# Performance work log

Measured on AMD Instinct MI355X. Metric: run time of the kernel, lower is better.

Reference implementation:

```python
import jax, jax.numpy as jnp
import numpy as np

B, P, K, D, T = 512, 64, 8, 512, 50000


def setup_inputs() -> dict:
    key = jax.random.key(0)
    k1, k2, k3, k4, k5, k6 = jax.random.split(key, 6)
    return {
        "inputs": jax.random.normal(k1, (B, P, D), dtype=jnp.float32),
        "title_emb_mat": jax.random.normal(k2, (T, D), dtype=jnp.float32),
        "nbr_batch": jax.random.randint(k3, (B, P, K), 0, B, dtype=jnp.int32),
        "nbr_job": jax.random.randint(k4, (B, P, K), 0, P, dtype=jnp.int32),
        "nbr_title": jax.random.randint(k5, (B, P, K), 0, T, dtype=jnp.int32),
        "nbr_mask": jax.random.randint(k6, (B, P, K), 0, 2, dtype=jnp.int32),
    }


def reference(inputs, title_emb_mat, nbr_batch, nbr_job, nbr_title, nbr_mask):
    # inputs:        [B, P, D]  job embeddings per employee position
    # title_emb_mat: [T, Dt]    title embedding table (Dt == D here)
    # nbr_*:         [B, P, K]  padded metapath neighbor indices + validity mask
    mask = nbr_mask.astype(bool)                              # [B,P,K]
    ref_embs = inputs[nbr_batch, nbr_job]                     # [B,P,K,D] gather of neighbor job embs
    # attention logits: focal emb vs neighbor embs (raw inner product, exp-normalized)
    raw_s = jnp.einsum('bpd,bpkd->bpk', inputs, ref_embs)     # [B,P,K]
    logits = jnp.where(mask, raw_s, jnp.float32(-1e9))
    sim = jax.nn.softmax(logits, axis=-1) * mask              # exact zeros on padded slots;
    # an all-masked (i,pos) -> uniform softmax * 0 mask == 0 row (matches torch 'continue' -> zeros)
    ref_t_embs = title_emb_mat[nbr_title]                     # [B,P,K,Dt] gather of target-title embs
    graph_concat = jnp.einsum('bpk,bpkt->bpt', sim, ref_t_embs)  # [B,P,Dt]
    out = jnp.concatenate([inputs, graph_concat], axis=-1)    # [B,P,D+Dt]
    return out.reshape(B * P, D + title_emb_mat.shape[1])     # torch.cat over batch, axis=0
```

## Files before the change

### kernel.cpp

```cpp
#include <hip/hip_runtime.h>

#define BB 512
#define PP 64
#define KK 8
#define DD 512

typedef float v4f __attribute__((ext_vector_type(4)));

__global__ __launch_bounds__(256) void han_meta_kernel(
    const float* __restrict__ inputs,
    const float* __restrict__ title,
    const int*   __restrict__ nbr_batch,
    const int*   __restrict__ nbr_job,
    const int*   __restrict__ nbr_title,
    const int*   __restrict__ nbr_mask,
    float*       __restrict__ out)
{
    const int lane = threadIdx.x & 63;
    const int wave = threadIdx.x >> 6;
    const int row  = blockIdx.x * 4 + wave;

    const float4* inp4 = (const float4*)(inputs + (size_t)row * DD);
    const float4 fa = inp4[lane];
    const float4 fb = inp4[lane + 64];

    const int4* nb4 = (const int4*)(nbr_batch + row * KK);
    const int4* nj4 = (const int4*)(nbr_job   + row * KK);
    const int4* nt4 = (const int4*)(nbr_title + row * KK);
    const int4* nm4 = (const int4*)(nbr_mask  + row * KK);
    int nbk[KK], njk[KK], ntk[KK], nmk[KK];
    *(int4*)&nbk[0] = nb4[0]; *(int4*)&nbk[4] = nb4[1];
    *(int4*)&njk[0] = nj4[0]; *(int4*)&njk[4] = nj4[1];
    *(int4*)&ntk[0] = nt4[0]; *(int4*)&ntk[4] = nt4[1];
    *(int4*)&nmk[0] = nm4[0]; *(int4*)&nmk[4] = nm4[1];

    float logit[KK];
    #pragma unroll
    for (int k = 0; k < KK; ++k) {
        if (nmk[k]) {
            const float4* g4 = (const float4*)(inputs +
                ((size_t)nbk[k] * PP + (size_t)njk[k]) * DD);
            const float4 ga = g4[lane];
            const float4 gb = g4[lane + 64];
            float d = fa.x*ga.x + fa.y*ga.y + fa.z*ga.z + fa.w*ga.w
                    + fb.x*gb.x + fb.y*gb.y + fb.z*gb.z + fb.w*gb.w;
            #pragma unroll
            for (int off = 32; off >= 1; off >>= 1)
                d += __shfl_xor(d, off, 64);
            logit[k] = d;
        } else {
            logit[k] = -1e9f;
        }
    }

    float m = logit[0];
    #pragma unroll
    for (int k = 1; k < KK; ++k) m = fmaxf(m, logit[k]);
    float e[KK];
    float s = 0.0f;
    #pragma unroll
    for (int k = 0; k < KK; ++k) {
        e[k] = expf(logit[k] - m);
        s += e[k];
    }
    const float inv = 1.0f / s;

    float4 oa = make_float4(0.f, 0.f, 0.f, 0.f);
    float4 ob = make_float4(0.f, 0.f, 0.f, 0.f);
    #pragma unroll
    for (int k = 0; k < KK; ++k) {
        if (nmk[k]) {
            const float w = e[k] * inv;
            const float4* t4 = (const float4*)(title + (size_t)ntk[k] * DD);
            const float4 ta = t4[lane];
            const float4 tb = t4[lane + 64];
            oa.x += w * ta.x; oa.y += w * ta.y; oa.z += w * ta.z; oa.w += w * ta.w;
            ob.x += w * tb.x; ob.y += w * tb.y; ob.z += w * tb.z; ob.w += w * tb.w;
        }
    }

    v4f* o4 = (v4f*)(out + (size_t)row * (2 * DD));
    v4f va = {fa.x, fa.y, fa.z, fa.w};
    v4f vb = {fb.x, fb.y, fb.z, fb.w};
    v4f vc = {oa.x, oa.y, oa.z, oa.w};
    v4f vd = {ob.x, ob.y, ob.z, ob.w};
    __builtin_nontemporal_store(va, o4 + lane);
    __builtin_nontemporal_store(vb, o4 + lane + 64);
    __builtin_nontemporal_store(vc, o4 + lane + 128);
    __builtin_nontemporal_store(vd, o4 + lane + 192);
}

extern "C" void kernel_launch(void* const* d_in, const int* in_sizes, int n_in,
                              void* d_out, int out_size, void* d_ws, size_t ws_size,
                              hipStream_t stream) {
    const float* inputs    = (const float*)d_in[0];
    const float* title     = (const float*)d_in[1];
    const int*   nbr_batch = (const int*)d_in[2];
    const int*   nbr_job   = (const int*)d_in[3];
    const int*   nbr_title = (const int*)d_in[4];
    const int*   nbr_mask  = (const int*)d_in[5];
    float*       out       = (float*)d_out;

    const int rows = BB * PP;
    dim3 grid(rows / 4);
    dim3 block(256);
    han_meta_kernel<<<grid, block, 0, stream>>>(
        inputs, title, nbr_batch, nbr_job, nbr_title, nbr_mask, out);
}
```

Baseline: 295.8 us.

## Split fused kernel into attention-weight and title-aggregation phases via workspace

Splits the single kernel into two launches. The first computes the softmax weights from the inputs gather and writes them to workspace along with the inputs half of the output. The second gathers title rows, weights them and writes the second half. The goal is to separate the two random-gather working sets so each phase gets better cache reuse. In exchange it adds a second launch and a small workspace round trip, and it falls back to the fused kernel if the workspace is too small.

```diff
diff --git a/kernel.cpp b/kernel.cpp
--- a/kernel.cpp
+++ b/kernel.cpp
@@ -7,14 +7,14 @@
 
 typedef float v4f __attribute__((ext_vector_type(4)));
 
-__global__ __launch_bounds__(256) void han_meta_kernel(
+
+__global__ __launch_bounds__(256) void han_phase1(
     const float* __restrict__ inputs,
-    const float* __restrict__ title,
     const int*   __restrict__ nbr_batch,
     const int*   __restrict__ nbr_job,
-    const int*   __restrict__ nbr_title,
     const int*   __restrict__ nbr_mask,
-    float*       __restrict__ out)
+    float*       __restrict__ out,
+    float*       __restrict__ sim)
 {
     const int lane = threadIdx.x & 63;
     const int wave = threadIdx.x >> 6;
@@ -26,12 +26,10 @@
 
     const int4* nb4 = (const int4*)(nbr_batch + row * KK);
     const int4* nj4 = (const int4*)(nbr_job   + row * KK);
-    const int4* nt4 = (const int4*)(nbr_title + row * KK);
     const int4* nm4 = (const int4*)(nbr_mask  + row * KK);
-    int nbk[KK], njk[KK], ntk[KK], nmk[KK];
+    int nbk[KK], njk[KK], nmk[KK];
     *(int4*)&nbk[0] = nb4[0]; *(int4*)&nbk[4] = nb4[1];
     *(int4*)&njk[0] = nj4[0]; *(int4*)&njk[4] = nj4[1];
-    *(int4*)&ntk[0] = nt4[0]; *(int4*)&ntk[4] = nt4[1];
     *(int4*)&nmk[0] = nm4[0]; *(int4*)&nmk[4] = nm4[1];
 
     float logit[KK];
@@ -65,6 +63,122 @@
     }
     const float inv = 1.0f / s;
 
+    v4f* o4 = (v4f*)(out + (size_t)row * (2 * DD));
+    v4f va = {fa.x, fa.y, fa.z, fa.w};
+    v4f vb = {fb.x, fb.y, fb.z, fb.w};
+    __builtin_nontemporal_store(va, o4 + lane);
+    __builtin_nontemporal_store(vb, o4 + lane + 64);
+
+    if (lane == 0) {
+        float4* s4 = (float4*)(sim + (size_t)row * KK);
+        s4[0] = make_float4(nmk[0] ? e[0]*inv : 0.f,
+                            nmk[1] ? e[1]*inv : 0.f,
+                            nmk[2] ? e[2]*inv : 0.f,
+                            nmk[3] ? e[3]*inv : 0.f);
+        s4[1] = make_float4(nmk[4] ? e[4]*inv : 0.f,
+                            nmk[5] ? e[5]*inv : 0.f,
+                            nmk[6] ? e[6]*inv : 0.f,
+                            nmk[7] ? e[7]*inv : 0.f);
+    }
+}
+
+__global__ __launch_bounds__(256) void han_phase2(
+    const float* __restrict__ title,
+    const int*   __restrict__ nbr_title,
+    const float* __restrict__ sim,
+    float*       __restrict__ out)
+{
+    const int lane = threadIdx.x & 63;
+    const int wave = threadIdx.x >> 6;
+    const int row  = blockIdx.x * 4 + wave;
+
+    const int4* nt4 = (const int4*)(nbr_title + row * KK);
+    int ntk[KK];
+    *(int4*)&ntk[0] = nt4[0]; *(int4*)&ntk[4] = nt4[1];
+
+    const float4* s4 = (const float4*)(sim + (size_t)row * KK);
+    const float4 w0 = s4[0];
+    const float4 w1 = s4[1];
+    const float w[KK] = {w0.x, w0.y, w0.z, w0.w, w1.x, w1.y, w1.z, w1.w};
+
+    float4 oa = make_float4(0.f, 0.f, 0.f, 0.f);
+    float4 ob = make_float4(0.f, 0.f, 0.f, 0.f);
+    #pragma unroll
+    for (int k = 0; k < KK; ++k) {
+        if (w[k] != 0.0f) {
+            const float4* t4 = (const float4*)(title + (size_t)ntk[k] * DD);
+            const float4 ta = t4[lane];
+            const float4 tb = t4[lane + 64];
+            oa.x += w[k]*ta.x; oa.y += w[k]*ta.y; oa.z += w[k]*ta.z; oa.w += w[k]*ta.w;
+            ob.x += w[k]*tb.x; ob.y += w[k]*tb.y; ob.z += w[k]*tb.z; ob.w += w[k]*tb.w;
+        }
+    }
+
+    v4f* o4 = (v4f*)(out + (size_t)row * (2 * DD));
+    v4f vc = {oa.x, oa.y, oa.z, oa.w};
+    v4f vd = {ob.x, ob.y, ob.z, ob.w};
+    __builtin_nontemporal_store(vc, o4 + lane + 128);
+    __builtin_nontemporal_store(vd, o4 + lane + 192);
+}
+
+__global__ __launch_bounds__(256) void han_meta_kernel(
+    const float* __restrict__ inputs,
+    const float* __restrict__ title,
+    const int*   __restrict__ nbr_batch,
+    const int*   __restrict__ nbr_job,
+    const int*   __restrict__ nbr_title,
+    const int*   __restrict__ nbr_mask,
+    float*       __restrict__ out)
+{
+    const int lane = threadIdx.x & 63;
+    const int wave = threadIdx.x >> 6;
+    const int row  = blockIdx.x * 4 + wave;
+
+    const float4* inp4 = (const float4*)(inputs + (size_t)row * DD);
+    const float4 fa = inp4[lane];
+    const float4 fb = inp4[lane + 64];
+
+    const int4* nb4 = (const int4*)(nbr_batch + row * KK);
+    const int4* nj4 = (const int4*)(nbr_job   + row * KK);
+    const int4* nt4 = (const int4*)(nbr_title + row * KK);
+    const int4* nm4 = (const int4*)(nbr_mask  + row * KK);
+    int nbk[KK], njk[KK], ntk[KK], nmk[KK];
+    *(int4*)&nbk[0] = nb4[0]; *(int4*)&nbk[4] = nb4[1];
+    *(int4*)&njk[0] = nj4[0]; *(int4*)&njk[4] = nj4[1];
+    *(int4*)&ntk[0] = nt4[0]; *(int4*)&ntk[4] = nt4[1];
+    *(int4*)&nmk[0] = nm4[0]; *(int4*)&nmk[4] = nm4[1];
+
+    float logit[KK];
+    #pragma unroll
+    for (int k = 0; k < KK; ++k) {
+        if (nmk[k]) {
+            const float4* g4 = (const float4*)(inputs +
+                ((size_t)nbk[k] * PP + (size_t)njk[k]) * DD);
+            const float4 ga = g4[lane];
+            const float4 gb = g4[lane + 64];
+            float d = fa.x*ga.x + fa.y*ga.y + fa.z*ga.z + fa.w*ga.w
+                    + fb.x*gb.x + fb.y*gb.y + fb.z*gb.z + fb.w*gb.w;
+            #pragma unroll
+            for (int off = 32; off >= 1; off >>= 1)
+                d += __shfl_xor(d, off, 64);
+            logit[k] = d;
+        } else {
+            logit[k] = -1e9f;
+        }
+    }
+
+    float m = logit[0];
+    #pragma unroll
+    for (int k = 1; k < KK; ++k) m = fmaxf(m, logit[k]);
+    float e[KK];
+    float s = 0.0f;
+    #pragma unroll
+    for (int k = 0; k < KK; ++k) {
+        e[k] = expf(logit[k] - m);
+        s += e[k];
+    }
+    const float inv = 1.0f / s;
+
     float4 oa = make_float4(0.f, 0.f, 0.f, 0.f);
     float4 ob = make_float4(0.f, 0.f, 0.f, 0.f);
     #pragma unroll
@@ -102,8 +216,19 @@
     float*       out       = (float*)d_out;
 
     const int rows = BB * PP;
+    const size_t sim_bytes = (size_t)rows * KK * sizeof(float);
+
     dim3 grid(rows / 4);
     dim3 block(256);
-    han_meta_kernel<<<grid, block, 0, stream>>>(
-        inputs, title, nbr_batch, nbr_job, nbr_title, nbr_mask, out);
-}
+
+    if (ws_size >= sim_bytes) {
+        float* sim = (float*)d_ws;
+        han_phase1<<<grid, block, 0, stream>>>(
+            inputs, nbr_batch, nbr_job, nbr_mask, out, sim);
+        han_phase2<<<grid, block, 0, stream>>>(
+            title, nbr_title, sim, out);
+    } else {
+        han_meta_kernel<<<grid, block, 0, stream>>>(
+            inputs, title, nbr_batch, nbr_job, nbr_title, nbr_mask, out);
+    }
+}
```

Result: slower. 305.1 us (+3.1%).

## Split into two kernels and batch all neighbor gathers for memory-level parallelism

Applied to the files above, without the earlier changes.

Splits the fused kernel into a phase that gathers neighbor job embeddings and computes softmax weights, and a phase that gathers title embeddings and forms the weighted sum. The weights are staged in the output buffer's second half. In each phase all eight neighbor rows are loaded up front, using a safe dummy address for masked slots, so loads can be in flight together instead of serialized behind branches. The shuffle reductions are also interleaved across the eight dot products. The cost is an extra kernel launch, more registers, and redundant loads for masked slots.

```diff
diff --git a/kernel.cpp b/kernel.cpp
--- a/kernel.cpp
+++ b/kernel.cpp
@@ -7,12 +7,11 @@
 
 typedef float v4f __attribute__((ext_vector_type(4)));
 
-__global__ __launch_bounds__(256) void han_meta_kernel(
+
+__global__ __launch_bounds__(256) void han_phase1(
     const float* __restrict__ inputs,
-    const float* __restrict__ title,
     const int*   __restrict__ nbr_batch,
     const int*   __restrict__ nbr_job,
-    const int*   __restrict__ nbr_title,
     const int*   __restrict__ nbr_mask,
     float*       __restrict__ out)
 {
@@ -20,38 +19,49 @@
     const int wave = threadIdx.x >> 6;
     const int row  = blockIdx.x * 4 + wave;
 
+    const int4* nb4 = (const int4*)(nbr_batch + row * KK);
+    const int4* nj4 = (const int4*)(nbr_job   + row * KK);
+    const int4* nm4 = (const int4*)(nbr_mask  + row * KK);
+    int nbk[KK], njk[KK], nmk[KK];
+    *(int4*)&nbk[0] = nb4[0]; *(int4*)&nbk[4] = nb4[1];
+    *(int4*)&njk[0] = nj4[0]; *(int4*)&njk[4] = nj4[1];
+    *(int4*)&nmk[0] = nm4[0]; *(int4*)&nmk[4] = nm4[1];
+
+    const float4* g4[KK];
+    #pragma unroll
+    for (int k = 0; k < KK; ++k) {
+        const size_t r = nmk[k] ? ((size_t)nbk[k] * PP + (size_t)njk[k])
+                                : (size_t)row;
+        g4[k] = (const float4*)(inputs + r * DD);
+    }
+
     const float4* inp4 = (const float4*)(inputs + (size_t)row * DD);
     const float4 fa = inp4[lane];
     const float4 fb = inp4[lane + 64];
+    float4 ga[KK], gb[KK];
+    #pragma unroll
+    for (int k = 0; k < KK; ++k) {
+        ga[k] = g4[k][lane];
+        gb[k] = g4[k][lane + 64];
+    }
 
-    const int4* nb4 = (const int4*)(nbr_batch + row * KK);
-    const int4* nj4 = (const int4*)(nbr_job   + row * KK);
-    const int4* nt4 = (const int4*)(nbr_title + row * KK);
-    const int4* nm4 = (const int4*)(nbr_mask  + row * KK);
-    int nbk[KK], njk[KK], ntk[KK], nmk[KK];
-    *(int4*)&nbk[0] = nb4[0]; *(int4*)&nbk[4] = nb4[1];
-    *(int4*)&njk[0] = nj4[0]; *(int4*)&njk[4] = nj4[1];
-    *(int4*)&ntk[0] = nt4[0]; *(int4*)&ntk[4] = nt4[1];
-    *(int4*)&nmk[0] = nm4[0]; *(int4*)&nmk[4] = nm4[1];
+    float d[KK];
+    #pragma unroll
+    for (int k = 0; k < KK; ++k) {
+        d[k] = fa.x*ga[k].x + fa.y*ga[k].y + fa.z*ga[k].z + fa.w*ga[k].w
+             + fb.x*gb[k].x + fb.y*gb[k].y + fb.z*gb[k].z + fb.w*gb[k].w;
+    }
+
+    #pragma unroll
+    for (int off = 32; off >= 1; off >>= 1) {
+        #pragma unroll
+        for (int k = 0; k < KK; ++k)
+            d[k] += __shfl_xor(d[k], off, 64);
+    }
 
     float logit[KK];
     #pragma unroll
-    for (int k = 0; k < KK; ++k) {
-        if (nmk[k]) {
-            const float4* g4 = (const float4*)(inputs +
-                ((size_t)nbk[k] * PP + (size_t)njk[k]) * DD);
-            const float4 ga = g4[lane];
-            const float4 gb = g4[lane + 64];
-            float d = fa.x*ga.x + fa.y*ga.y + fa.z*ga.z + fa.w*ga.w
-                    + fb.x*gb.x + fb.y*gb.y + fb.z*gb.z + fb.w*gb.w;
-            #pragma unroll
-            for (int off = 32; off >= 1; off >>= 1)
-                d += __shfl_xor(d, off, 64);
-            logit[k] = d;
-        } else {
-            logit[k] = -1e9f;
-        }
-    }
+    for (int k = 0; k < KK; ++k) logit[k] = nmk[k] ? d[k] : -1e9f;
 
     float m = logit[0];
     #pragma unroll
@@ -65,27 +75,73 @@
     }
     const float inv = 1.0f / s;
 
+    v4f* o4 = (v4f*)(out + (size_t)row * (2 * DD));
+    v4f va = {fa.x, fa.y, fa.z, fa.w};
+    v4f vb = {fb.x, fb.y, fb.z, fb.w};
+    __builtin_nontemporal_store(va, o4 + lane);
+    __builtin_nontemporal_store(vb, o4 + lane + 64);
+
+    if (lane == 0) {
+        float4* s4 = (float4*)(out + (size_t)row * (2 * DD) + DD);
+        s4[0] = make_float4(nmk[0] ? e[0]*inv : 0.f,
+                            nmk[1] ? e[1]*inv : 0.f,
+                            nmk[2] ? e[2]*inv : 0.f,
+                            nmk[3] ? e[3]*inv : 0.f);
+        s4[1] = make_float4(nmk[4] ? e[4]*inv : 0.f,
+                            nmk[5] ? e[5]*inv : 0.f,
+                            nmk[6] ? e[6]*inv : 0.f,
+                            nmk[7] ? e[7]*inv : 0.f);
+    }
+}
+
+__global__ __launch_bounds__(256) void han_phase2(
+    const float* __restrict__ title,
+    const int*   __restrict__ nbr_title,
+    const int*   __restrict__ nbr_mask,
+    float*       __restrict__ out)
+{
+    const int lane = threadIdx.x & 63;
+    const int wave = threadIdx.x >> 6;
+    const int row  = blockIdx.x * 4 + wave;
+
+    const int4* nt4 = (const int4*)(nbr_title + row * KK);
+    const int4* nm4 = (const int4*)(nbr_mask  + row * KK);
+    int ntk[KK], nmk[KK];
+    *(int4*)&ntk[0] = nt4[0]; *(int4*)&ntk[4] = nt4[1];
+    *(int4*)&nmk[0] = nm4[0]; *(int4*)&nmk[4] = nm4[1];
+
+    const float4* t4[KK];
+    #pragma unroll
+    for (int k = 0; k < KK; ++k) {
+        const size_t r = nmk[k] ? (size_t)ntk[k] : (size_t)0;
+        t4[k] = (const float4*)(title + r * DD);
+    }
+
+    float4 ta[KK], tb[KK];
+    #pragma unroll
+    for (int k = 0; k < KK; ++k) {
+        ta[k] = t4[k][lane];
+        tb[k] = t4[k][lane + 64];
+    }
+
+    const float4* s4 = (const float4*)(out + (size_t)row * (2 * DD) + DD);
+    const float4 w0 = s4[0];
+    const float4 w1 = s4[1];
+    const float w[KK] = {w0.x, w0.y, w0.z, w0.w, w1.x, w1.y, w1.z, w1.w};
+
     float4 oa = make_float4(0.f, 0.f, 0.f, 0.f);
     float4 ob = make_float4(0.f, 0.f, 0.f, 0.f);
     #pragma unroll
     for (int k = 0; k < KK; ++k) {
-        if (nmk[k]) {
-            const float w = e[k] * inv;
-            const float4* t4 = (const float4*)(title + (size_t)ntk[k] * DD);
-            const float4 ta = t4[lane];
-            const float4 tb = t4[lane + 64];
-            oa.x += w * ta.x; oa.y += w * ta.y; oa.z += w * ta.z; oa.w += w * ta.w;
-            ob.x += w * tb.x; ob.y += w * tb.y; ob.z += w * tb.z; ob.w += w * tb.w;
-        }
+        oa.x += w[k]*ta[k].x; oa.y += w[k]*ta[k].y;
+        oa.z += w[k]*ta[k].z; oa.w += w[k]*ta[k].w;
+        ob.x += w[k]*tb[k].x; ob.y += w[k]*tb[k].y;
+        ob.z += w[k]*tb[k].z; ob.w += w[k]*tb[k].w;
     }
 
     v4f* o4 = (v4f*)(out + (size_t)row * (2 * DD));
-    v4f va = {fa.x, fa.y, fa.z, fa.w};
-    v4f vb = {fb.x, fb.y, fb.z, fb.w};
     v4f vc = {oa.x, oa.y, oa.z, oa.w};
     v4f vd = {ob.x, ob.y, ob.z, ob.w};
-    __builtin_nontemporal_store(va, o4 + lane);
-    __builtin_nontemporal_store(vb, o4 + lane + 64);
     __builtin_nontemporal_store(vc, o4 + lane + 128);
     __builtin_nontemporal_store(vd, o4 + lane + 192);
 }
@@ -104,6 +160,9 @@
     const int rows = BB * PP;
     dim3 grid(rows / 4);
     dim3 block(256);
-    han_meta_kernel<<<grid, block, 0, stream>>>(
-        inputs, title, nbr_batch, nbr_job, nbr_title, nbr_mask, out);
+
+    han_phase1<<<grid, block, 0, stream>>>(
+        inputs, nbr_batch, nbr_job, nbr_mask, out);
+    han_phase2<<<grid, block, 0, stream>>>(
+        title, nbr_title, nbr_mask, out);
 }
```

New measurement: 309.3 us. 1.05x slower.
